# Kernel tuning notes

Measured on AMD Instinct MI355X. Metric: run time of the kernel, lower is better.

Reference implementation:

```python
import jax, jax.numpy as jnp
import numpy as np

# Dims: module math forces per-head depth D == num_points == N (see analysis).
B, H, N = 4, 8, 1024
D = N                      # q_depth = k_depth = v_depth = num_points
C_IN = 64                  # q_in = k_in = v_in
C_OUT = H * D              # q_out = k_out = v_out = 8192
SCALE = float(np.sqrt(D))


def _split_heads(t):
    # t: [B, C_OUT, N] -> view(B, H, D, N) -> permute -> [B, H, N, D]
    return t.reshape(B, H, D, N).transpose(0, 1, 3, 2)


def setup_inputs() -> dict:
    key = jax.random.key(0)
    ks = jax.random.split(key, 9)
    s = 0.02
    return {
        "coordinate": jax.random.normal(ks[0], (B, 3, N), jnp.float32),
        "x": jax.random.normal(ks[1], (B, C_IN, N, 1), jnp.float32),
        "neighbors": jax.random.normal(ks[2], (B, C_IN, N, 1), jnp.float32),
        # 1x1 Conv2d weights (out, in), no bias
        "Wq": jax.random.normal(ks[3], (C_OUT, C_IN), jnp.float32) * s,
        "Wk": jax.random.normal(ks[4], (C_OUT, C_IN), jnp.float32) * s,
        "Wv": jax.random.normal(ks[5], (C_OUT, C_IN), jnp.float32) * s,
        # nn.Linear(3, q_out) / nn.Linear(3, v_out)
        "Wlq": jax.random.normal(ks[6], (C_OUT, 3), jnp.float32) * s,
        "blq": jnp.zeros((C_OUT,), jnp.float32),
        "Wlv": jax.random.normal(ks[7], (C_OUT, 3), jnp.float32) * s,
        "blv": jnp.zeros((C_OUT,), jnp.float32),
    }


def reference(coordinate, x, neighbors, Wq, Wk, Wv, Wlq, blq, Wlv, blv):
    # Att_Score_method='dot_product', pos_method='method_ii' (hardcoded branch)
    xs = x[..., 0]           # [B, C_IN, N]  (squeeze trailing Conv2d width dim)
    ns = neighbors[..., 0]   # [B, C_IN, N]

    q = _split_heads(jnp.einsum('oc,bcn->bon', Wq, xs))  # [B,H,N,D]
    k = _split_heads(jnp.einsum('oc,bcn->bon', Wk, ns))  # [B,H,N,D]
    v = _split_heads(jnp.einsum('oc,bcn->bon', Wv, ns))  # [B,H,N,D]

    coords = coordinate.transpose(0, 2, 1)               # [B, N, 3]
    # positional encodings, split into heads: [B,H,N,D]
    pos_q = _split_heads((coords @ Wlq.T + blq).transpose(0, 2, 1))
    pos_v = _split_heads((coords @ Wlv.T + blv).transpose(0, 2, 1))

    # q_context = q @ pos_q^T ; energy = q @ k^T + q_context  -> [B,H,N,N]
    q_context = jnp.einsum('bhnd,bhmd->bhnm', q, pos_q)
    energy = jnp.einsum('bhnd,bhmd->bhnm', q, k) + q_context

    attn = jax.nn.softmax(energy / SCALE, axis=-1)       # [B,H,N,N]
    v_context = v + pos_v                                 # [B,H,N,D], D==N
    out = attn * v_context                                # elementwise combine

    # permute(0,2,1,3) -> [B,N,H,D] -> reshape [B,N,H*D] -> permute -> [B,H*D,N]
    out = out.transpose(0, 2, 1, 3).reshape(B, N, H * D).transpose(0, 2, 1)
    return out
```

## Files before the change

### kernel.cpp

```cpp
#include <hip/hip_runtime.h>

#define NN 1024
#define KP 96
#define LSTR 104

typedef __attribute__((ext_vector_type(8))) short short8;
typedef __attribute__((ext_vector_type(4))) short short4v;
typedef __attribute__((ext_vector_type(4))) float f32x4;

__device__ __forceinline__ short f2bf(float f){
  unsigned u = __builtin_bit_cast(unsigned, f);
  u += 0x7FFFu + ((u >> 16) & 1u);
  return (short)(u >> 16);
}

__global__ __launch_bounds__(1024) void k_prep_pt(
    const float* __restrict__ Wq, const float* __restrict__ Wk,
    const float* __restrict__ Wlq, const float* __restrict__ blq,
    float* __restrict__ PTf){
  int t = threadIdx.x, c = t & 63, p = t >> 6;
  int h = blockIdx.y, kk0 = blockIdx.x * 8, dz = blockIdx.z;
  float acc[8];
  #pragma unroll
  for (int i = 0; i < 8; ++i) acc[i] = 0.f;
  #pragma unroll
  for (int i = 0; i < 16; ++i){
    int o = h * 1024 + p * 64 + dz * 16 + i;
    float wq = Wq[o * 64 + c];
    #pragma unroll
    for (int j = 0; j < 8; ++j){
      int kk = kk0 + j;
      float bv;
      if (kk < 64)        bv = Wk[o * 64 + kk];
      else if (kk < 67)   bv = Wlq[o * 3 + (kk - 64)];
      else if (kk == 67)  bv = blq[o];
      else                bv = 0.f;
      acc[j] += wq * bv;
    }
  }
  __shared__ float red[16][64][8];
  #pragma unroll
  for (int j = 0; j < 8; ++j) red[p][c][j] = acc[j];
  __syncthreads();
  if (p == 0){
    #pragma unroll
    for (int j = 0; j < 8; ++j){
      float s = 0.f;
      for (int pp = 0; pp < 16; ++pp) s += red[pp][c][j];
      atomicAdd(&PTf[(h * KP + kk0 + j) * 64 + c], s);
    }
  }
}

__global__ __launch_bounds__(256) void k_prep_b(
    const float* __restrict__ ns, const float* __restrict__ coord,
    short* __restrict__ Bm){
  int t = threadIdx.x;
  int b = blockIdx.y, m0 = blockIdx.x * 64;
  __shared__ float nsT[64][65];
  __shared__ float cst[3][64];
  #pragma unroll
  for (int it = 0; it < 16; ++it){
    int idx = it * 256 + t;
    int c = idx >> 6, mm = idx & 63;
    nsT[mm][c] = ns[(b * 64 + c) * NN + m0 + mm];
  }
  if (t < 192){
    int j = t >> 6, mm = t & 63;
    cst[j][mm] = coord[(b * 3 + j) * NN + m0 + mm];
  }
  __syncthreads();
  #pragma unroll
  for (int it = 0; it < 24; ++it){
    int idx = it * 256 + t;
    int mm = idx / KP, kk = idx - mm * KP;
    float v = (kk < 64) ? nsT[mm][kk]
            : (kk < 67) ? cst[kk - 64][mm]
            : (kk == 67) ? 1.f : 0.f;
    Bm[(b * NN + m0 + mm) * KP + kk] = f2bf(v);
  }
}

__global__ __launch_bounds__(256) void k_prep_v(
    const float* __restrict__ Wv, const float* __restrict__ Wlv,
    const float* __restrict__ blv, short* __restrict__ Vm){
  int t = threadIdx.x, o0 = blockIdx.x * 64;
  #pragma unroll
  for (int it = 0; it < 24; ++it){
    int idx = it * 256 + t;
    int r = idx / KP, kk = idx - r * KP;
    int o = o0 + r;
    float v = (kk < 64) ? Wv[o * 64 + kk]
            : (kk < 67) ? Wlv[o * 3 + (kk - 64)]
            : (kk == 67) ? blv[o] : 0.f;
    Vm[o * KP + kk] = f2bf(v);
  }
}

__global__ __launch_bounds__(256) void attn_main(
    const float* __restrict__ xs, const float* __restrict__ PTf,
    const short* __restrict__ Bmat, const short* __restrict__ Vm,
    float* __restrict__ out){
  __shared__ short xsL[64 * 64];
  __shared__ short AL[64 * LSTR];
  __shared__ float redS[64 * 4];
  const int t = threadIdx.x, w = t >> 6, lane = t & 63;
  const int q = lane >> 4, ln = lane & 15;
  const int blk = blockIdx.x, nb = blk & 15, bh = blk >> 4;
  const int b = bh >> 3, h = bh & 7;
  const int n0 = nb * 64;

  const float* xsb = xs + b * 64 * NN;
  #pragma unroll
  for (int it = 0; it < 4; ++it){
    int idx = it * 256 + t;
    int c = idx >> 4, nn4 = (idx & 15) << 2;
    f32x4 v = *(const f32x4*)(xsb + c * NN + n0 + nn4);
    short4v pk;
    #pragma unroll
    for (int j = 0; j < 4; ++j) pk[j] = f2bf(v[j]);
    *(short4v*)(&xsL[c * 64 + nn4]) = pk;
  }
  __syncthreads();

  short8 xf0, xf1;
  #pragma unroll
  for (int j = 0; j < 8; ++j){
    xf0[j] = xsL[(q * 8 + j) * 64 + w * 16 + ln];
    xf1[j] = xsL[(32 + q * 8 + j) * 64 + w * 16 + ln];
  }
  const float* PTh = PTf + h * KP * 64;
  #pragma unroll
  for (int kt = 0; kt < 6; ++kt){
    const float* pr = PTh + (kt * 16 + ln) * 64;
    f32x4 pa = *(const f32x4*)(pr + q * 8);
    f32x4 pb = *(const f32x4*)(pr + q * 8 + 4);
    f32x4 pc = *(const f32x4*)(pr + 32 + q * 8);
    f32x4 pd = *(const f32x4*)(pr + 32 + q * 8 + 4);
    short8 p0, p1;
    #pragma unroll
    for (int j = 0; j < 4; ++j){
      p0[j] = f2bf(pa[j]); p0[4 + j] = f2bf(pb[j]);
      p1[j] = f2bf(pc[j]); p1[4 + j] = f2bf(pd[j]);
    }
    f32x4 a = {0.f, 0.f, 0.f, 0.f};
    a = __builtin_amdgcn_mfma_f32_16x16x32_bf16(xf0, p0, a, 0, 0, 0);
    a = __builtin_amdgcn_mfma_f32_16x16x32_bf16(xf1, p1, a, 0, 0, 0);
    #pragma unroll
    for (int r = 0; r < 4; ++r)
      AL[(w * 16 + q * 4 + r) * LSTR + kt * 16 + ln] = f2bf(a[r]);
  }
  __syncthreads();

  short8 af[4][3], bn[4][3];
  const short* Bb = Bmat + b * NN * KP;
  #pragma unroll
  for (int rf = 0; rf < 4; ++rf){
    #pragma unroll
    for (int s = 0; s < 3; ++s){
      af[rf][s] = *(const short8*)(&AL[(rf * 16 + ln) * LSTR + s * 32 + q * 8]);
      bn[rf][s] = *(const short8*)(Bb + (n0 + rf * 16 + ln) * KP + s * 32 + q * 8);
    }
  }
  const float KEXP = 0.045084220f;

  float sum[4][4];
  #pragma unroll
  for (int rf = 0; rf < 4; ++rf)
    #pragma unroll
    for (int r = 0; r < 4; ++r) sum[rf][r] = 0.f;

  short8 bf0, bf1, bf2;
  {
    const short* bp = Bb + (w * 256 + ln) * KP + q * 8;
    bf0 = *(const short8*)(bp);
    bf1 = *(const short8*)(bp + 32);
    bf2 = *(const short8*)(bp + 64);
  }
  for (int ms = 0; ms < 16; ++ms){
    short8 nb0, nb1, nb2;
    {
      int msn = (ms + 1) & 15;
      const short* bp = Bb + (w * 256 + msn * 16 + ln) * KP + q * 8;
      nb0 = *(const short8*)(bp);
      nb1 = *(const short8*)(bp + 32);
      nb2 = *(const short8*)(bp + 64);
    }
    #pragma unroll
    for (int rf = 0; rf < 4; ++rf){
      f32x4 e = {0.f, 0.f, 0.f, 0.f};
      e = __builtin_amdgcn_mfma_f32_16x16x32_bf16(af[rf][0], bf0, e, 0, 0, 0);
      e = __builtin_amdgcn_mfma_f32_16x16x32_bf16(af[rf][1], bf1, e, 0, 0, 0);
      e = __builtin_amdgcn_mfma_f32_16x16x32_bf16(af[rf][2], bf2, e, 0, 0, 0);
      #pragma unroll
      for (int r = 0; r < 4; ++r)
        sum[rf][r] += __builtin_amdgcn_exp2f(e[r] * KEXP);
    }
    bf0 = nb0; bf1 = nb1; bf2 = nb2;
  }
  #pragma unroll
  for (int rf = 0; rf < 4; ++rf){
    #pragma unroll
    for (int r = 0; r < 4; ++r){
      float s = sum[rf][r];
      s += __shfl_xor(s, 1); s += __shfl_xor(s, 2);
      s += __shfl_xor(s, 4); s += __shfl_xor(s, 8);
      sum[rf][r] = s;
    }
  }
  if (ln == 0){
    #pragma unroll
    for (int rf = 0; rf < 4; ++rf)
      #pragma unroll
      for (int r = 0; r < 4; ++r)
        redS[(rf * 16 + q * 4 + r) * 4 + w] = sum[rf][r];
  }
  __syncthreads();
  float rinv[4][4];
  #pragma unroll
  for (int rf = 0; rf < 4; ++rf){
    #pragma unroll
    for (int r = 0; r < 4; ++r){
      f32x4 v4 = *(const f32x4*)(&redS[(rf * 16 + q * 4 + r) * 4]);
      rinv[rf][r] = 1.0f / (v4[0] + v4[1] + v4[2] + v4[3]);
    }
  }

  float* outp = out + (size_t)bh * (1024 * 1024);
  const short* Vh = Vm + h * 1024 * KP;
  short8 vf0, vf1, vf2;
  {
    const short* bp = Bb + (w * 256 + ln) * KP + q * 8;
    const short* vp = Vh + (w * 256 + ln) * KP + q * 8;
    bf0 = *(const short8*)(bp); bf1 = *(const short8*)(bp + 32); bf2 = *(const short8*)(bp + 64);
    vf0 = *(const short8*)(vp); vf1 = *(const short8*)(vp + 32); vf2 = *(const short8*)(vp + 64);
  }
  for (int ds = 0; ds < 16; ++ds){
    int d0 = w * 256 + ds * 16;
    short8 nb0, nb1, nb2, nv0, nv1, nv2;
    {
      int dsn = (ds + 1) & 15;
      const short* bp = Bb + (w * 256 + dsn * 16 + ln) * KP + q * 8;
      const short* vp = Vh + (w * 256 + dsn * 16 + ln) * KP + q * 8;
      nb0 = *(const short8*)(bp); nb1 = *(const short8*)(bp + 32); nb2 = *(const short8*)(bp + 64);
      nv0 = *(const short8*)(vp); nv1 = *(const short8*)(vp + 32); nv2 = *(const short8*)(vp + 64);
    }
    #pragma unroll
    for (int rf = 0; rf < 4; ++rf){
      f32x4 e  = {0.f, 0.f, 0.f, 0.f};
      f32x4 vv = {0.f, 0.f, 0.f, 0.f};
      e  = __builtin_amdgcn_mfma_f32_16x16x32_bf16(af[rf][0], bf0, e, 0, 0, 0);
      e  = __builtin_amdgcn_mfma_f32_16x16x32_bf16(af[rf][1], bf1, e, 0, 0, 0);
      e  = __builtin_amdgcn_mfma_f32_16x16x32_bf16(af[rf][2], bf2, e, 0, 0, 0);
      vv = __builtin_amdgcn_mfma_f32_16x16x32_bf16(bn[rf][0], vf0, vv, 0, 0, 0);
      vv = __builtin_amdgcn_mfma_f32_16x16x32_bf16(bn[rf][1], vf1, vv, 0, 0, 0);
      vv = __builtin_amdgcn_mfma_f32_16x16x32_bf16(bn[rf][2], vf2, vv, 0, 0, 0);
      f32x4 o;
      #pragma unroll
      for (int r = 0; r < 4; ++r)
        o[r] = __builtin_amdgcn_exp2f(e[r] * KEXP) * rinv[rf][r] * vv[r];
      *(f32x4*)(outp + (d0 + ln) * NN + n0 + rf * 16 + q * 4) = o;
    }
    bf0 = nb0; bf1 = nb1; bf2 = nb2;
    vf0 = nv0; vf1 = nv1; vf2 = nv2;
  }
}

extern "C" void kernel_launch(void* const* d_in, const int* in_sizes, int n_in,
                              void* d_out, int out_size, void* d_ws, size_t ws_size,
                              hipStream_t stream){
  const float* coord = (const float*)d_in[0];
  const float* x     = (const float*)d_in[1];
  const float* nbr   = (const float*)d_in[2];
  const float* Wq    = (const float*)d_in[3];
  const float* Wk    = (const float*)d_in[4];
  const float* Wv    = (const float*)d_in[5];
  const float* Wlq   = (const float*)d_in[6];
  const float* blq   = (const float*)d_in[7];
  const float* Wlv   = (const float*)d_in[8];
  const float* blv   = (const float*)d_in[9];
  float* out = (float*)d_out;

  char* ws = (char*)d_ws;
  float* PTf = (float*)ws;
  short* Bm  = (short*)(ws + 196608);
  short* Vm  = (short*)(ws + 196608 + 786432);

  hipMemsetAsync(PTf, 0, 196608, stream);
  k_prep_pt<<<dim3(12, 8, 4), 1024, 0, stream>>>(Wq, Wk, Wlq, blq, PTf);
  k_prep_b <<<dim3(16, 4),     256, 0, stream>>>(nbr, coord, Bm);
  k_prep_v <<<128,             256, 0, stream>>>(Wv, Wlv, blv, Vm);
  attn_main<<<512,             256, 0, stream>>>(x, PTf, Bm, Vm, out);
}
```

Measured before the change: 247.4 us.

## Merge prep kernels, cache softmax numerators, and store PT precomputed in bf16

Folds the three prep kernels and the memset into one launch that writes the PT product directly in bf16, with no atomics. In the main kernel, exp(energy) values are kept in registers per row-fragment so the second pass no longer recomputes the energy MFMAs. The loop over row fragments is restructured, with a block sync per fragment, launch bounds allowing two blocks per unit, and nontemporal output stores. This cuts redundant MFMA work and launch overhead, but adds register pressure from the 16-entry P array and extra barriers.

After: 296.8 us. 20.0% more time.

```diff
diff --git a/kernel.cpp b/kernel.cpp
--- a/kernel.cpp
+++ b/kernel.cpp
@@ -14,96 +14,110 @@
   return (short)(u >> 16);
 }
 
-__global__ __launch_bounds__(1024) void k_prep_pt(
+__global__ __launch_bounds__(256) void prep_all(
     const float* __restrict__ Wq, const float* __restrict__ Wk,
     const float* __restrict__ Wlq, const float* __restrict__ blq,
-    float* __restrict__ PTf){
-  int t = threadIdx.x, c = t & 63, p = t >> 6;
-  int h = blockIdx.y, kk0 = blockIdx.x * 8, dz = blockIdx.z;
-  float acc[8];
-  #pragma unroll
-  for (int i = 0; i < 8; ++i) acc[i] = 0.f;
-  #pragma unroll
-  for (int i = 0; i < 16; ++i){
-    int o = h * 1024 + p * 64 + dz * 16 + i;
-    float wq = Wq[o * 64 + c];
-    #pragma unroll
-    for (int j = 0; j < 8; ++j){
-      int kk = kk0 + j;
-      float bv;
-      if (kk < 64)        bv = Wk[o * 64 + kk];
-      else if (kk < 67)   bv = Wlq[o * 3 + (kk - 64)];
-      else if (kk == 67)  bv = blq[o];
-      else                bv = 0.f;
-      acc[j] += wq * bv;
-    }
-  }
-  __shared__ float red[16][64][8];
-  #pragma unroll
-  for (int j = 0; j < 8; ++j) red[p][c][j] = acc[j];
-  __syncthreads();
-  if (p == 0){
-    #pragma unroll
-    for (int j = 0; j < 8; ++j){
-      float s = 0.f;
-      for (int pp = 0; pp < 16; ++pp) s += red[pp][c][j];
-      atomicAdd(&PTf[(h * KP + kk0 + j) * 64 + c], s);
-    }
-  }
-}
-
-__global__ __launch_bounds__(256) void k_prep_b(
     const float* __restrict__ ns, const float* __restrict__ coord,
-    short* __restrict__ Bm){
-  int t = threadIdx.x;
-  int b = blockIdx.y, m0 = blockIdx.x * 64;
-  __shared__ float nsT[64][65];
-  __shared__ float cst[3][64];
-  #pragma unroll
-  for (int it = 0; it < 16; ++it){
-    int idx = it * 256 + t;
-    int c = idx >> 6, mm = idx & 63;
-    nsT[mm][c] = ns[(b * 64 + c) * NN + m0 + mm];
-  }
-  if (t < 192){
-    int j = t >> 6, mm = t & 63;
-    cst[j][mm] = coord[(b * 3 + j) * NN + m0 + mm];
-  }
-  __syncthreads();
-  #pragma unroll
-  for (int it = 0; it < 24; ++it){
-    int idx = it * 256 + t;
-    int mm = idx / KP, kk = idx - mm * KP;
-    float v = (kk < 64) ? nsT[mm][kk]
-            : (kk < 67) ? cst[kk - 64][mm]
-            : (kk == 67) ? 1.f : 0.f;
-    Bm[(b * NN + m0 + mm) * KP + kk] = f2bf(v);
-  }
-}
-
-__global__ __launch_bounds__(256) void k_prep_v(
     const float* __restrict__ Wv, const float* __restrict__ Wlv,
-    const float* __restrict__ blv, short* __restrict__ Vm){
-  int t = threadIdx.x, o0 = blockIdx.x * 64;
-  #pragma unroll
-  for (int it = 0; it < 24; ++it){
-    int idx = it * 256 + t;
-    int r = idx / KP, kk = idx - r * KP;
-    int o = o0 + r;
-    float v = (kk < 64) ? Wv[o * 64 + kk]
-            : (kk < 67) ? Wlv[o * 3 + (kk - 64)]
-            : (kk == 67) ? blv[o] : 0.f;
-    Vm[o * KP + kk] = f2bf(v);
-  }
-}
-
-__global__ __launch_bounds__(256) void attn_main(
-    const float* __restrict__ xs, const float* __restrict__ PTf,
+    const float* __restrict__ blv,
+    short* __restrict__ PTbf, short* __restrict__ Bm, short* __restrict__ Vm){
+  __shared__ union SU {
+    float red[4][64][9];
+    struct { float nsT[64][65]; float cst[3][64]; } bb;
+  } S;
+  const int t = threadIdx.x;
+  const int r = blockIdx.x;
+
+  if (r < 96){
+    const int h = r / 12, kidx = r % 12, kk0 = kidx * 8;
+    const int c = t & 63, p = t >> 6;
+    if (kidx > 8){
+      if (p == 0){
+        #pragma unroll
+        for (int j = 0; j < 8; ++j) PTbf[(h*96 + kk0 + j)*64 + c] = 0;
+      }
+      return;
+    }
+    float acc[8];
+    #pragma unroll
+    for (int j = 0; j < 8; ++j) acc[j] = 0.f;
+    if (kidx < 8){
+      #pragma unroll 4
+      for (int i = 0; i < 256; ++i){
+        const int o = h*1024 + p*256 + i;
+        const float wq = Wq[o*64 + c];
+        const float* wk = Wk + o*64 + kk0;
+        f32x4 b0 = *(const f32x4*)(wk);
+        f32x4 b1 = *(const f32x4*)(wk + 4);
+        #pragma unroll
+        for (int j = 0; j < 4; ++j){ acc[j] += wq*b0[j]; acc[4+j] += wq*b1[j]; }
+      }
+    } else {
+      #pragma unroll 4
+      for (int i = 0; i < 256; ++i){
+        const int o = h*1024 + p*256 + i;
+        const float wq = Wq[o*64 + c];
+        acc[0] += wq * Wlq[o*3 + 0];
+        acc[1] += wq * Wlq[o*3 + 1];
+        acc[2] += wq * Wlq[o*3 + 2];
+        acc[3] += wq * blq[o];
+      }
+    }
+    #pragma unroll
+    for (int j = 0; j < 8; ++j) S.red[p][c][j] = acc[j];
+    __syncthreads();
+    if (p == 0){
+      #pragma unroll
+      for (int j = 0; j < 8; ++j){
+        float s = S.red[0][c][j] + S.red[1][c][j] + S.red[2][c][j] + S.red[3][c][j];
+        PTbf[(h*96 + kk0 + j)*64 + c] = f2bf(s);
+      }
+    }
+  } else if (r < 160){
+    const int rb = r - 96;
+    const int b = rb >> 4, m0 = (rb & 15) * 64;
+    #pragma unroll
+    for (int it = 0; it < 16; ++it){
+      int idx = it * 256 + t;
+      int c = idx >> 6, mm = idx & 63;
+      S.bb.nsT[mm][c] = ns[(b*64 + c)*NN + m0 + mm];
+    }
+    if (t < 192){
+      int j = t >> 6, mm = t & 63;
+      S.bb.cst[j][mm] = coord[(b*3 + j)*NN + m0 + mm];
+    }
+    __syncthreads();
+    #pragma unroll
+    for (int it = 0; it < 24; ++it){
+      int idx = it * 256 + t;
+      int mm = idx / KP, kk = idx - mm*KP;
+      float v = (kk < 64) ? S.bb.nsT[mm][kk]
+              : (kk < 67) ? S.bb.cst[kk - 64][mm]
+              : (kk == 67) ? 1.f : 0.f;
+      Bm[(b*NN + m0 + mm)*KP + kk] = f2bf(v);
+    }
+  } else {
+    const int o0 = (r - 160) * 64;
+    #pragma unroll
+    for (int it = 0; it < 24; ++it){
+      int idx = it * 256 + t;
+      int rr = idx / KP, kk = idx - rr*KP;
+      int o = o0 + rr;
+      float v = (kk < 64) ? Wv[o*64 + kk]
+              : (kk < 67) ? Wlv[o*3 + (kk - 64)]
+              : (kk == 67) ? blv[o] : 0.f;
+      Vm[o*KP + kk] = f2bf(v);
+    }
+  }
+}
+
+__global__ __launch_bounds__(256, 2) void attn_main(
+    const float* __restrict__ xs, const short* __restrict__ PTbf,
     const short* __restrict__ Bmat, const short* __restrict__ Vm,
     float* __restrict__ out){
   __shared__ short xsL[64 * 64];
   __shared__ short AL[64 * LSTR];
-  __shared__ float redS[64 * 4];
+  __shared__ float redS[16 * 4];
   const int t = threadIdx.x, w = t >> 6, lane = t & 63;
   const int q = lane >> 4, ln = lane & 15;
   const int blk = blockIdx.x, nb = blk & 15, bh = blk >> 4;
@@ -129,140 +143,111 @@
     xf0[j] = xsL[(q * 8 + j) * 64 + w * 16 + ln];
     xf1[j] = xsL[(32 + q * 8 + j) * 64 + w * 16 + ln];
   }
-  const float* PTh = PTf + h * KP * 64;
+  const short* PTh = PTbf + h * 96 * 64;
   #pragma unroll
   for (int kt = 0; kt < 6; ++kt){
-    const float* pr = PTh + (kt * 16 + ln) * 64;
-    f32x4 pa = *(const f32x4*)(pr + q * 8);
-    f32x4 pb = *(const f32x4*)(pr + q * 8 + 4);
-    f32x4 pc = *(const f32x4*)(pr + 32 + q * 8);
-    f32x4 pd = *(const f32x4*)(pr + 32 + q * 8 + 4);
-    short8 p0, p1;
-    #pragma unroll
-    for (int j = 0; j < 4; ++j){
-      p0[j] = f2bf(pa[j]); p0[4 + j] = f2bf(pb[j]);
-      p1[j] = f2bf(pc[j]); p1[4 + j] = f2bf(pd[j]);
-    }
+    const short* pr = PTh + (kt * 16 + ln) * 64;
+    short8 p0 = *(const short8*)(pr + q * 8);
+    short8 p1 = *(const short8*)(pr + 32 + q * 8);
     f32x4 a = {0.f, 0.f, 0.f, 0.f};
     a = __builtin_amdgcn_mfma_f32_16x16x32_bf16(xf0, p0, a, 0, 0, 0);
     a = __builtin_amdgcn_mfma_f32_16x16x32_bf16(xf1, p1, a, 0, 0, 0);
     #pragma unroll
-    for (int r = 0; r < 4; ++r)
-      AL[(w * 16 + q * 4 + r) * LSTR + kt * 16 + ln] = f2bf(a[r]);
+    for (int rr = 0; rr < 4; ++rr)
+      AL[(w * 16 + q * 4 + rr) * LSTR + kt * 16 + ln] = f2bf(a[rr]);
   }
   __syncthreads();
 
-  short8 af[4][3], bn[4][3];
   const short* Bb = Bmat + b * NN * KP;
-  #pragma unroll
+  const short* Vh = Vm + h * 1024 * KP;
+  float* outp = out + (size_t)bh * (1024 * 1024);
+  const float KEXP = 0.045084220f;
+
   for (int rf = 0; rf < 4; ++rf){
-    #pragma unroll
-    for (int s = 0; s < 3; ++s){
-      af[rf][s] = *(const short8*)(&AL[(rf * 16 + ln) * LSTR + s * 32 + q * 8]);
-      bn[rf][s] = *(const short8*)(Bb + (n0 + rf * 16 + ln) * KP + s * 32 + q * 8);
-    }
-  }
-  const float KEXP = 0.045084220f;
-
-  float sum[4][4];
-  #pragma unroll
-  for (int rf = 0; rf < 4; ++rf)
-    #pragma unroll
-    for (int r = 0; r < 4; ++r) sum[rf][r] = 0.f;
-
-  short8 bf0, bf1, bf2;
-  {
-    const short* bp = Bb + (w * 256 + ln) * KP + q * 8;
-    bf0 = *(const short8*)(bp);
-    bf1 = *(const short8*)(bp + 32);
-    bf2 = *(const short8*)(bp + 64);
-  }
-  for (int ms = 0; ms < 16; ++ms){
-    short8 nb0, nb1, nb2;
+    const short* ap = &AL[(rf * 16 + ln) * LSTR + q * 8];
+    short8 af0 = *(const short8*)(ap);
+    short8 af1 = *(const short8*)(ap + 32);
+    short8 af2 = *(const short8*)(ap + 64);
+
+    f32x4 P[16];
+    f32x4 sum = {0.f, 0.f, 0.f, 0.f};
+    short8 bf0, bf1, bf2;
     {
-      int msn = (ms + 1) & 15;
-      const short* bp = Bb + (w * 256 + msn * 16 + ln) * KP + q * 8;
-      nb0 = *(const short8*)(bp);
-      nb1 = *(const short8*)(bp + 32);
-      nb2 = *(const short8*)(bp + 64);
-    }
-    #pragma unroll
-    for (int rf = 0; rf < 4; ++rf){
+      const short* bp = Bb + (w * 256 + ln) * KP + q * 8;
+      bf0 = *(const short8*)(bp);
+      bf1 = *(const short8*)(bp + 32);
+      bf2 = *(const short8*)(bp + 64);
+    }
+    #pragma unroll
+    for (int ms = 0; ms < 16; ++ms){
+      short8 nb0, nb1, nb2;
+      {
+        int msn = (ms + 1) & 15;
+        const short* bp = Bb + (w * 256 + msn * 16 + ln) * KP + q * 8;
+        nb0 = *(const short8*)(bp);
+        nb1 = *(const short8*)(bp + 32);
+        nb2 = *(const short8*)(bp + 64);
+      }
       f32x4 e = {0.f, 0.f, 0.f, 0.f};
-      e = __builtin_amdgcn_mfma_f32_16x16x32_bf16(af[rf][0], bf0, e, 0, 0, 0);
-      e = __builtin_amdgcn_mfma_f32_16x16x32_bf16(af[rf][1], bf1, e, 0, 0, 0);
-      e = __builtin_amdgcn_mfma_f32_16x16x32_bf16(af[rf][2], bf2, e, 0, 0, 0);
+      e = __builtin_amdgcn_mfma_f32_16x16x32_bf16(af0, bf0, e, 0, 0, 0);
+      e = __builtin_amdgcn_mfma_f32_16x16x32_bf16(af1, bf1, e, 0, 0, 0);
+      e = __builtin_amdgcn_mfma_f32_16x16x32_bf16(af2, bf2, e, 0, 0, 0);
+      f32x4 p;
       #pragma unroll
-      for (int r = 0; r < 4; ++r)
-        sum[rf][r] += __builtin_amdgcn_exp2f(e[r] * KEXP);
-    }
-    bf0 = nb0; bf1 = nb1; bf2 = nb2;
-  }
-  #pragma unroll
-  for (int rf = 0; rf < 4; ++rf){
-    #pragma unroll
-    for (int r = 0; r < 4; ++r){
-      float s = sum[rf][r];
+      for (int rr = 0; rr < 4; ++rr) p[rr] = __builtin_amdgcn_exp2f(e[rr] * KEXP);
+      P[ms] = p;
+      sum += p;
+      bf0 = nb0; bf1 = nb1; bf2 = nb2;
+    }
+    #pragma unroll
+    for (int rr = 0; rr < 4; ++rr){
+      float s = sum[rr];
       s += __shfl_xor(s, 1); s += __shfl_xor(s, 2);
       s += __shfl_xor(s, 4); s += __shfl_xor(s, 8);
-      sum[rf][r] = s;
-    }
-  }
-  if (ln == 0){
-    #pragma unroll
-    for (int rf = 0; rf < 4; ++rf)
-      #pragma unroll
-      for (int r = 0; r < 4; ++r)
-        redS[(rf * 16 + q * 4 + r) * 4 + w] = sum[rf][r];
-  }
-  __syncthreads();
-  float rinv[4][4];
-  #pragma unroll
-  for (int rf = 0; rf < 4; ++rf){
-    #pragma unroll
-    for (int r = 0; r < 4; ++r){
-      f32x4 v4 = *(const f32x4*)(&redS[(rf * 16 + q * 4 + r) * 4]);
-      rinv[rf][r] = 1.0f / (v4[0] + v4[1] + v4[2] + v4[3]);
-    }
-  }
-
-  float* outp = out + (size_t)bh * (1024 * 1024);
-  const short* Vh = Vm + h * 1024 * KP;
-  short8 vf0, vf1, vf2;
-  {
-    const short* bp = Bb + (w * 256 + ln) * KP + q * 8;
-    const short* vp = Vh + (w * 256 + ln) * KP + q * 8;
-    bf0 = *(const short8*)(bp); bf1 = *(const short8*)(bp + 32); bf2 = *(const short8*)(bp + 64);
-    vf0 = *(const short8*)(vp); vf1 = *(const short8*)(vp + 32); vf2 = *(const short8*)(vp + 64);
-  }
-  for (int ds = 0; ds < 16; ++ds){
-    int d0 = w * 256 + ds * 16;
-    short8 nb0, nb1, nb2, nv0, nv1, nv2;
+      if (ln == 0) redS[(q * 4 + rr) * 4 + w] = s;
+    }
+    __syncthreads();
+    f32x4 rinv;
+    #pragma unroll
+    for (int rr = 0; rr < 4; ++rr){
+      f32x4 v4 = *(const f32x4*)(&redS[(q * 4 + rr) * 4]);
+      rinv[rr] = 1.0f / (v4[0] + v4[1] + v4[2] + v4[3]);
+    }
+
+    const short* np = Bb + (n0 + rf * 16 + ln) * KP + q * 8;
+    short8 bn0 = *(const short8*)(np);
+    short8 bn1 = *(const short8*)(np + 32);
+    short8 bn2 = *(const short8*)(np + 64);
+    short8 vf0, vf1, vf2;
     {
-      int dsn = (ds + 1) & 15;
-      const short* bp = Bb + (w * 256 + dsn * 16 + ln) * KP + q * 8;
-      const short* vp = Vh + (w * 256 + dsn * 16 + ln) * KP + q * 8;
-      nb0 = *(const short8*)(bp); nb1 = *(const short8*)(bp + 32); nb2 = *(const short8*)(bp + 64);
-      nv0 = *(const short8*)(vp); nv1 = *(const short8*)(vp + 32); nv2 = *(const short8*)(vp + 64);
-    }
-    #pragma unroll
-    for (int rf = 0; rf < 4; ++rf){
-      f32x4 e  = {0.f, 0.f, 0.f, 0.f};
+      const short* vp = Vh + (w * 256 + ln) * KP + q * 8;
+      vf0 = *(const short8*)(vp);
+      vf1 = *(const short8*)(vp + 32);
+      vf2 = *(const short8*)(vp + 64);
+    }
+    #pragma unroll
+    for (int ds = 0; ds < 16; ++ds){
+      int d0 = w * 256 + ds * 16;
+      short8 nv0, nv1, nv2;
+      {
+        int dsn = (ds + 1) & 15;
+        const short* vp = Vh + (w * 256 + dsn * 16 + ln) * KP + q * 8;
+        nv0 = *(const short8*)(vp);
+        nv1 = *(const short8*)(vp + 32);
+        nv2 = *(const short8*)(vp + 64);
+      }
       f32x4 vv = {0.f, 0.f, 0.f, 0.f};
-      e  = __builtin_amdgcn_mfma_f32_16x16x32_bf16(af[rf][0], bf0, e, 0, 0, 0);
-      e  = __builtin_amdgcn_mfma_f32_16x16x32_bf16(af[rf][1], bf1, e, 0, 0, 0);
-      e  = __builtin_amdgcn_mfma_f32_16x16x32_bf16(af[rf][2], bf2, e, 0, 0, 0);
-      vv = __builtin_amdgcn_mfma_f32_16x16x32_bf16(bn[rf][0], vf0, vv, 0, 0, 0);
-      vv = __builtin_amdgcn_mfma_f32_16x16x32_bf16(bn[rf][1], vf1, vv, 0, 0, 0);
-      vv = __builtin_amdgcn_mfma_f32_16x16x32_bf16(bn[rf][2], vf2, vv, 0, 0, 0);
+      vv = __builtin_amdgcn_mfma_f32_16x16x32_bf16(bn0, vf0, vv, 0, 0, 0);
+      vv = __builtin_amdgcn_mfma_f32_16x16x32_bf16(bn1, vf1, vv, 0, 0, 0);
+      vv = __builtin_amdgcn_mfma_f32_16x16x32_bf16(bn2, vf2, vv, 0, 0, 0);
       f32x4 o;
       #pragma unroll
-      for (int r = 0; r < 4; ++r)
-        o[r] = __builtin_amdgcn_exp2f(e[r] * KEXP) * rinv[rf][r] * vv[r];
-      *(f32x4*)(outp + (d0 + ln) * NN + n0 + rf * 16 + q * 4) = o;
-    }
-    bf0 = nb0; bf1 = nb1; bf2 = nb2;
-    vf0 = nv0; vf1 = nv1; vf2 = nv2;
+      for (int rr = 0; rr < 4; ++rr)
+        o[rr] = P[ds][rr] * rinv[rr] * vv[rr];
+      __builtin_nontemporal_store(o, (f32x4*)(outp + (d0 + ln) * NN + n0 + rf * 16 + q * 4));
+      vf0 = nv0; vf1 = nv1; vf2 = nv2;
+    }
+    __syncthreads();
   }
 }
 
@@ -282,13 +267,11 @@
   float* out = (float*)d_out;
 
   char* ws = (char*)d_ws;
-  float* PTf = (float*)ws;
-  short* Bm  = (short*)(ws + 196608);
-  short* Vm  = (short*)(ws + 196608 + 786432);
-
-  hipMemsetAsync(PTf, 0, 196608, stream);
-  k_prep_pt<<<dim3(12, 8, 4), 1024, 0, stream>>>(Wq, Wk, Wlq, blq, PTf);
-  k_prep_b <<<dim3(16, 4),     256, 0, stream>>>(nbr, coord, Bm);
-  k_prep_v <<<128,             256, 0, stream>>>(Wv, Wlv, blv, Vm);
-  attn_main<<<512,             256, 0, stream>>>(x, PTf, Bm, Vm, out);
-}
+  short* PTbf = (short*)ws;
+  short* Bm   = (short*)(ws + 98304);
+  short* Vm   = (short*)(ws + 98304 + 786432);
+
+  prep_all<<<288, 256, 0, stream>>>(Wq, Wk, Wlq, blq, nbr, coord, Wv, Wlv, blv,
+                                    PTbf, Bm, Vm);
+  attn_main<<<512, 256, 0, stream>>>(x, PTbf, Bm, Vm, out);
+}
```
